# Performance work log

Measured on AMD Instinct MI355X. Metric: run time of the kernel, lower is better.

Reference implementation:

```python
import jax, jax.numpy as jnp
import numpy as np

M, C = 100000, 24
LINE_W, LENGTH_W, REPROJ_W = 0.0, 0.0, 1.0  # forward() default weights


def setup_inputs() -> dict:
    ks = jax.random.split(jax.random.key(0), 8)
    # 3 pole markers per frame, centered ~5m in front of cameras (positive depth)
    pole3d = 0.5 * jax.random.normal(ks[0], (M, 3, 3), jnp.float32) + jnp.array([0.0, 0.0, 5.0], jnp.float32)
    # intrinsics: fx=fy~1000, principal point ~(960,540)
    fx = 1000.0 + 10.0 * jax.random.normal(ks[1], (C,), jnp.float32)
    fy = 1000.0 + 10.0 * jax.random.normal(ks[2], (C,), jnp.float32)
    u0 = 960.0 + 5.0 * jax.random.normal(ks[3], (C,), jnp.float32)
    v0 = 540.0 + 5.0 * jax.random.normal(ks[4], (C,), jnp.float32)
    K = jnp.zeros((C, 3, 3), jnp.float32)
    K = K.at[:, 0, 0].set(fx).at[:, 1, 1].set(fy).at[:, 0, 2].set(u0).at[:, 1, 2].set(v0).at[:, 2, 2].set(1.0)
    dist = 0.01 * jax.random.normal(ks[5], (C, 5), jnp.float32)  # k1,k2,p1,p2,k3
    R = jnp.eye(3, dtype=jnp.float32)[None] + 0.01 * jax.random.normal(ks[6], (C, 3, 3), jnp.float32)
    t = 0.1 * jax.random.normal(ks[7], (C, 3), jnp.float32)
    # detected pixels in a 1920x1080 frame
    pole2d = jax.random.uniform(jax.random.fold_in(ks[0], 1), (M, C, 3, 2), jnp.float32) * jnp.array([1920.0, 1080.0], jnp.float32)
    # visibility mask; guarantee >=1 visible camera per frame (matches non-empty loss_reproj)
    mask = jax.random.randint(jax.random.fold_in(ks[0], 2), (M, C), 0, 2, jnp.int32).at[:, 0].set(1)
    pole = jnp.array([0.5, 0.5], jnp.float32)  # [d1, d2] in meters
    return {"pole3d": pole3d, "pole2d": pole2d, "K": K, "dist": dist, "R": R, "t": t, "pole": pole, "mask": mask}


def _project(X, K, R, t, dist):
    # X: [M,P,3] world points; outputs pixels [M,C,P,2]
    xc = jnp.einsum('cij,mpj->mcpi', R, X) + t[None, :, None, :]   # camera frame
    xn = xc[..., :2] / xc[..., 2:3]                                # perspective divide
    x0, x1 = xn[..., 0], xn[..., 1]
    r2 = x0 * x0 + x1 * x1
    k1, k2, p1, p2, k3 = (dist[:, i][None, :, None] for i in range(5))
    radial = 1.0 + k1 * r2 + k2 * r2 * r2 + k3 * r2 * r2 * r2
    xu = x0 * radial + 2.0 * p1 * x0 * x1 + p2 * (r2 + 2.0 * x0 * x0)
    yu = x1 * radial + p1 * (r2 + 2.0 * x1 * x1) + 2.0 * p2 * x0 * x1
    fx = K[:, 0, 0][None, :, None]; fy = K[:, 1, 1][None, :, None]
    u0 = K[:, 0, 2][None, :, None]; v0 = K[:, 1, 2][None, :, None]
    return jnp.stack([fx * xu + u0, fy * yu + v0], axis=-1)


def reference(pole3d, pole2d, K, dist, R, t, pole, mask):
    d1, d2 = pole[0], pole[1]
    dsum = d1 + d2
    # wand geometry loss per frame
    expect_mid = (d2 * pole3d[:, 0] + d1 * pole3d[:, 2]) / dsum            # [M,3]
    loss_line = jnp.linalg.norm(pole3d[:, 1] - expect_mid, axis=-1)        # [M]
    loss_length = jnp.abs(jnp.linalg.norm(pole3d[:, 0] - pole3d[:, 2], axis=-1) - dsum)
    loss_wand = LINE_W * loss_line + LENGTH_W * loss_length                # [M]
    # reprojection loss
    proj = _project(pole3d, K, R, t, dist)                                 # [M,C,3,2]
    per_cam = REPROJ_W * jnp.linalg.norm(pole2d - proj, axis=-1).mean(axis=-1)  # [M,C]
    m = mask.astype(per_cam.dtype)
    loss_reproj = (per_cam * m).sum(axis=-1) / m.sum(axis=-1)              # masked mean over cams
    return jnp.mean(loss_wand + loss_reproj)
```

## Files before the change

### kernel.cpp

```cpp
#include <hip/hip_runtime.h>

#define MM 100000
#define CC 24
#define BLK 256
#define WPB (BLK / 64)
#define GRID 1280
#define NW (GRID * WPB)
#define NP (MM / 2)

struct Pack {
    float2 a0, a1, a2;
    float  w;
    float  q[9];
};

__device__ __forceinline__ Pack load_pack(
    const float* __restrict__ pole3d, const float* __restrict__ pole2d,
    const int* __restrict__ mask, int m, int c, float active)
{
    Pack pk;
    const float2* pd = (const float2*)(pole2d + ((size_t)m * CC + c) * 6);
    pk.a0 = pd[0]; pk.a1 = pd[1]; pk.a2 = pd[2];
    pk.w = active * (float)mask[(size_t)m * CC + c];
    const float* q = pole3d + (size_t)m * 9;
    #pragma unroll
    for (int i = 0; i < 9; ++i) pk.q[i] = q[i];
    return pk;
}

__global__ __launch_bounds__(BLK) void ba_main_kernel(
    const float* __restrict__ pole3d,
    const float* __restrict__ pole2d,
    const float* __restrict__ Kmat,
    const float* __restrict__ dist,
    const float* __restrict__ Rmat,
    const float* __restrict__ tvec,
    const int*   __restrict__ mask,
    float* __restrict__ ws)
{
    const int tid  = threadIdx.x;
    const int lane = tid & 63;
    const int half = lane >> 5;
    const int cl   = lane & 31;
    const int c    = (cl < CC) ? cl : (CC - 1);
    const float active = (cl < CC) ? 1.f : 0.f;

    const float fx = Kmat[c * 9 + 0], fy = Kmat[c * 9 + 4];
    const float u0 = Kmat[c * 9 + 2], v0 = Kmat[c * 9 + 5];
    const float k1 = dist[c * 5 + 0], k2 = dist[c * 5 + 1];
    const float p1 = dist[c * 5 + 2], p2 = dist[c * 5 + 3], k3 = dist[c * 5 + 4];
    const float r00 = Rmat[c * 9 + 0], r01 = Rmat[c * 9 + 1], r02 = Rmat[c * 9 + 2];
    const float r10 = Rmat[c * 9 + 3], r11 = Rmat[c * 9 + 4], r12 = Rmat[c * 9 + 5];
    const float r20 = Rmat[c * 9 + 6], r21 = Rmat[c * 9 + 7], r22 = Rmat[c * 9 + 8];
    const float t0 = tvec[c * 3 + 0], t1 = tvec[c * 3 + 1], t2 = tvec[c * 3 + 2];

    const int wid = blockIdx.x * WPB + (tid >> 6);

    float acc = 0.f;

    Pack cur = load_pack(pole3d, pole2d, mask, 2 * wid + half, c, active);

    for (int p = wid; p < NP; p += NW) {
        const int pn = p + NW;
        const int pc = (pn < NP) ? pn : wid;
        Pack nxt = load_pack(pole3d, pole2d, mask, 2 * pc + half, c, active);

        float s = 0.f;
        const float2 obs[3] = {cur.a0, cur.a1, cur.a2};
        #pragma unroll
        for (int i = 0; i < 3; ++i) {
            const float X = cur.q[3 * i + 0], Y = cur.q[3 * i + 1], Z = cur.q[3 * i + 2];
            const float xc = r00 * X + r01 * Y + r02 * Z + t0;
            const float yc = r10 * X + r11 * Y + r12 * Z + t1;
            const float zc = r20 * X + r21 * Y + r22 * Z + t2;
            const float inv = __builtin_amdgcn_rcpf(zc);
            const float x0 = xc * inv, x1 = yc * inv;
            const float r2 = x0 * x0 + x1 * x1;
            const float radial = 1.f + r2 * (k1 + r2 * (k2 + r2 * k3));
            const float xu = x0 * radial + 2.f * p1 * x0 * x1 + p2 * (r2 + 2.f * x0 * x0);
            const float yu = x1 * radial + p1 * (r2 + 2.f * x1 * x1) + 2.f * p2 * x0 * x1;
            const float u = fx * xu + u0;
            const float v = fy * yu + v0;
            const float dx = obs[i].x - u;
            const float dy = obs[i].y - v;
            s += __builtin_amdgcn_sqrtf(dx * dx + dy * dy);
        }
        s *= (1.f / 3.f);

        float ss = s * cur.w;
        float ww = cur.w;
        #pragma unroll
        for (int d = 1; d < 32; d <<= 1) {
            ss += __shfl_xor(ss, d);
            ww += __shfl_xor(ww, d);
        }
        acc += ss * __builtin_amdgcn_rcpf(ww);

        cur = nxt;
    }

    float tot = acc + __shfl_xor(acc, 32);

    __shared__ float sh[WPB];
    if (lane == 0) sh[tid >> 6] = tot;
    __syncthreads();
    if (tid == 0) {
        float bl = 0.f;
        #pragma unroll
        for (int j = 0; j < WPB; ++j) bl += sh[j];
        ws[blockIdx.x] = bl;
    }
}

__global__ __launch_bounds__(256) void ba_reduce_kernel(
    const float* __restrict__ ws, float* __restrict__ out)
{
    __shared__ float sh[256];
    float s = 0.f;
    for (int i = threadIdx.x; i < GRID; i += 256) s += ws[i];
    sh[threadIdx.x] = s;
    __syncthreads();
    #pragma unroll
    for (int st = 128; st > 0; st >>= 1) {
        if (threadIdx.x < st) sh[threadIdx.x] += sh[threadIdx.x + st];
        __syncthreads();
    }
    if (threadIdx.x == 0) out[0] = sh[0] * (1.0f / MM);
}

extern "C" void kernel_launch(void* const* d_in, const int* in_sizes, int n_in,
                              void* d_out, int out_size, void* d_ws, size_t ws_size,
                              hipStream_t stream) {
    const float* pole3d = (const float*)d_in[0];
    const float* pole2d = (const float*)d_in[1];
    const float* Kmat   = (const float*)d_in[2];
    const float* dist   = (const float*)d_in[3];
    const float* Rmat   = (const float*)d_in[4];
    const float* tvec   = (const float*)d_in[5];
    const int*   mask   = (const int*)d_in[7];
    float* out = (float*)d_out;
    float* ws  = (float*)d_ws;

    ba_main_kernel<<<GRID, BLK, 0, stream>>>(
        pole3d, pole2d, Kmat, dist, Rmat, tvec, mask, ws);
    ba_reduce_kernel<<<1, 256, 0, stream>>>(ws, out);
}
```

Measured before the change: 28.51 us.

## Share pole3d via bpermute, double-depth prefetch, fuse final reduction with atomic counter

Each lane now loads only one pole3d scalar and the nine coordinates are broadcast within each half-wave via ds_bpermute, cutting redundant loads. The main loop processes two frame-pairs per iteration with two packs prefetched ahead to deepen memory-level parallelism. The separate reduction kernel is replaced by a last-block-done pattern using an atomic counter in workspace, reset by a memset, saving a launch at the cost of an atomic and fences.

```diff
diff --git a/kernel.cpp b/kernel.cpp
--- a/kernel.cpp
+++ b/kernel.cpp
@@ -8,23 +8,19 @@
 #define NW (GRID * WPB)
 #define NP (MM / 2)
 
-struct Pack {
-    float2 a0, a1, a2;
-    float  w;
-    float  q[9];
-};
+struct Pack { float2 a0, a1, a2; float w; float qv; };
 
 __device__ __forceinline__ Pack load_pack(
     const float* __restrict__ pole3d, const float* __restrict__ pole2d,
-    const int* __restrict__ mask, int m, int c, float active)
+    const int* __restrict__ mask, int m, int c, int cl, float active)
 {
     Pack pk;
     const float2* pd = (const float2*)(pole2d + ((size_t)m * CC + c) * 6);
     pk.a0 = pd[0]; pk.a1 = pd[1]; pk.a2 = pd[2];
-    pk.w = active * (float)mask[(size_t)m * CC + c];
-    const float* q = pole3d + (size_t)m * 9;
-    #pragma unroll
-    for (int i = 0; i < 9; ++i) pk.q[i] = q[i];
+    pk.w  = active * (float)mask[(size_t)m * CC + c];
+    float qv = 0.f;
+    if (cl < 9) qv = pole3d[(size_t)m * 9 + cl];
+    pk.qv = qv;
     return pk;
 }
 
@@ -36,7 +32,8 @@
     const float* __restrict__ Rmat,
     const float* __restrict__ tvec,
     const int*   __restrict__ mask,
-    float* __restrict__ ws)
+    float* __restrict__ ws,
+    float* __restrict__ out)
 {
     const int tid  = threadIdx.x;
     const int lane = tid & 63;
@@ -44,6 +41,7 @@
     const int cl   = lane & 31;
     const int c    = (cl < CC) ? cl : (CC - 1);
     const float active = (cl < CC) ? 1.f : 0.f;
+    const int qbase = half * 128;
 
     const float fx = Kmat[c * 9 + 0], fy = Kmat[c * 9 + 4];
     const float u0 = Kmat[c * 9 + 2], v0 = Kmat[c * 9 + 5];
@@ -58,18 +56,17 @@
 
     float acc = 0.f;
 
-    Pack cur = load_pack(pole3d, pole2d, mask, 2 * wid + half, c, active);
-
-    for (int p = wid; p < NP; p += NW) {
-        const int pn = p + NW;
-        const int pc = (pn < NP) ? pn : wid;
-        Pack nxt = load_pack(pole3d, pole2d, mask, 2 * pc + half, c, active);
-
+    auto consume = [&](const Pack& pk) {
+        float q[9];
+        #pragma unroll
+        for (int i = 0; i < 9; ++i)
+            q[i] = __int_as_float(__builtin_amdgcn_ds_bpermute(
+                       qbase + 4 * i, __float_as_int(pk.qv)));
+        const float2 obs[3] = {pk.a0, pk.a1, pk.a2};
         float s = 0.f;
-        const float2 obs[3] = {cur.a0, cur.a1, cur.a2};
         #pragma unroll
         for (int i = 0; i < 3; ++i) {
-            const float X = cur.q[3 * i + 0], Y = cur.q[3 * i + 1], Z = cur.q[3 * i + 2];
+            const float X = q[3 * i + 0], Y = q[3 * i + 1], Z = q[3 * i + 2];
             const float xc = r00 * X + r01 * Y + r02 * Z + t0;
             const float yc = r10 * X + r11 * Y + r12 * Z + t1;
             const float zc = r20 * X + r21 * Y + r22 * Z + t2;
@@ -86,46 +83,55 @@
             s += __builtin_amdgcn_sqrtf(dx * dx + dy * dy);
         }
         s *= (1.f / 3.f);
-
-        float ss = s * cur.w;
-        float ww = cur.w;
+        float ss = s * pk.w, ww = pk.w;
         #pragma unroll
         for (int d = 1; d < 32; d <<= 1) {
             ss += __shfl_xor(ss, d);
             ww += __shfl_xor(ww, d);
         }
         acc += ss * __builtin_amdgcn_rcpf(ww);
+    };
 
-        cur = nxt;
+    Pack c0 = load_pack(pole3d, pole2d, mask, 2 * wid + half, c, cl, active);
+    Pack c1 = load_pack(pole3d, pole2d, mask, 2 * (wid + NW) + half, c, cl, active);
+
+    for (int p = wid; p < NP; p += 2 * NW) {
+        const int p2 = p + 2 * NW, p3 = p + 3 * NW;
+        Pack n0{}, n1{};
+        if (p2 < NP) n0 = load_pack(pole3d, pole2d, mask, 2 * p2 + half, c, cl, active);
+        if (p3 < NP) n1 = load_pack(pole3d, pole2d, mask, 2 * p3 + half, c, cl, active);
+        consume(c0);
+        if (p + NW < NP) consume(c1);
+        c0 = n0; c1 = n1;
     }
 
-    float tot = acc + __shfl_xor(acc, 32);
+    const float tot = acc + __shfl_xor(acc, 32);
 
     __shared__ float sh[WPB];
+    __shared__ int lastFlag;
     if (lane == 0) sh[tid >> 6] = tot;
     __syncthreads();
+
+    float* partials = ws + 64;
     if (tid == 0) {
         float bl = 0.f;
         #pragma unroll
         for (int j = 0; j < WPB; ++j) bl += sh[j];
-        ws[blockIdx.x] = bl;
+        partials[blockIdx.x] = bl;
+        __threadfence();
+        const unsigned prev = atomicAdd((unsigned*)ws, 1u);
+        lastFlag = (prev == GRID - 1);
     }
-}
+    __syncthreads();
 
-__global__ __launch_bounds__(256) void ba_reduce_kernel(
-    const float* __restrict__ ws, float* __restrict__ out)
-{
-    __shared__ float sh[256];
-    float s = 0.f;
-    for (int i = threadIdx.x; i < GRID; i += 256) s += ws[i];
-    sh[threadIdx.x] = s;
-    __syncthreads();
-    #pragma unroll
-    for (int st = 128; st > 0; st >>= 1) {
-        if (threadIdx.x < st) sh[threadIdx.x] += sh[threadIdx.x + st];
-        __syncthreads();
+    if (lastFlag && tid < 64) {
+        __threadfence();
+        float s = 0.f;
+        for (int i = tid; i < GRID; i += 64) s += partials[i];
+        #pragma unroll
+        for (int d = 1; d < 64; d <<= 1) s += __shfl_xor(s, d);
+        if (tid == 0) out[0] = s * (1.0f / MM);
     }
-    if (threadIdx.x == 0) out[0] = sh[0] * (1.0f / MM);
 }
 
 extern "C" void kernel_launch(void* const* d_in, const int* in_sizes, int n_in,
@@ -141,7 +147,8 @@
     float* out = (float*)d_out;
     float* ws  = (float*)d_ws;
 
+    hipMemsetAsync(ws, 0, sizeof(unsigned), stream);
+
     ba_main_kernel<<<GRID, BLK, 0, stream>>>(
-        pole3d, pole2d, Kmat, dist, Rmat, tvec, mask, ws);
-    ba_reduce_kernel<<<1, 256, 0, stream>>>(ws, out);
+        pole3d, pole2d, Kmat, dist, Rmat, tvec, mask, ws, out);
 }
```

Measured after the change: 60.26 us. 111% more time.

## Fuse final reduction via last-block atomic counter and use ballot for mask counts

Applied to the files above, without the earlier changes.

The separate reduce kernel is removed. Each block now writes its partial sum and bumps an atomic counter, and the last block to finish sums all partials and writes the output. The per-frame visible-camera count is taken with a ballot plus popcount instead of a second shuffle reduction. The grid shrinks and launch bounds gain an occupancy hint. A memset is added before the launch to reset the counter, which costs an extra stream operation, and the threadfence/atomic pattern adds a little tail latency.

```diff
diff --git a/kernel.cpp b/kernel.cpp
--- a/kernel.cpp
+++ b/kernel.cpp
@@ -4,7 +4,7 @@
 #define CC 24
 #define BLK 256
 #define WPB (BLK / 64)
-#define GRID 1280
+#define GRID 1024
 #define NW (GRID * WPB)
 #define NP (MM / 2)
 
@@ -21,14 +21,14 @@
     Pack pk;
     const float2* pd = (const float2*)(pole2d + ((size_t)m * CC + c) * 6);
     pk.a0 = pd[0]; pk.a1 = pd[1]; pk.a2 = pd[2];
-    pk.w = active * (float)mask[(size_t)m * CC + c];
+    pk.w  = active * (float)mask[(size_t)m * CC + c];
     const float* q = pole3d + (size_t)m * 9;
     #pragma unroll
     for (int i = 0; i < 9; ++i) pk.q[i] = q[i];
     return pk;
 }
 
-__global__ __launch_bounds__(BLK) void ba_main_kernel(
+__global__ __launch_bounds__(BLK, 4) void ba_main_kernel(
     const float* __restrict__ pole3d,
     const float* __restrict__ pole2d,
     const float* __restrict__ Kmat,
@@ -36,7 +36,8 @@
     const float* __restrict__ Rmat,
     const float* __restrict__ tvec,
     const int*   __restrict__ mask,
-    float* __restrict__ ws)
+    float* __restrict__ ws,
+    float* __restrict__ out)
 {
     const int tid  = threadIdx.x;
     const int lane = tid & 63;
@@ -87,45 +88,47 @@
         }
         s *= (1.f / 3.f);
 
+        const unsigned long long ball = __ballot(cur.w != 0.f);
+        const unsigned wcnt = half ? __popcll(ball >> 32)
+                                   : __popcll(ball & 0xFFFFFFFFull);
+        const float ww = (float)wcnt;
+
         float ss = s * cur.w;
-        float ww = cur.w;
         #pragma unroll
-        for (int d = 1; d < 32; d <<= 1) {
-            ss += __shfl_xor(ss, d);
-            ww += __shfl_xor(ww, d);
-        }
+        for (int d = 1; d < 32; d <<= 1) ss += __shfl_xor(ss, d);
+
         acc += ss * __builtin_amdgcn_rcpf(ww);
 
         cur = nxt;
     }
 
-    float tot = acc + __shfl_xor(acc, 32);
+    const float tot = acc + __shfl_xor(acc, 32);
 
     __shared__ float sh[WPB];
+    __shared__ int lastFlag;
     if (lane == 0) sh[tid >> 6] = tot;
     __syncthreads();
+
+    float* partials = ws + 64;
     if (tid == 0) {
         float bl = 0.f;
         #pragma unroll
         for (int j = 0; j < WPB; ++j) bl += sh[j];
-        ws[blockIdx.x] = bl;
+        partials[blockIdx.x] = bl;
+        __threadfence();
+        const unsigned prev = atomicAdd((unsigned*)ws, 1u);
+        lastFlag = (prev == GRID - 1);
     }
-}
+    __syncthreads();
 
-__global__ __launch_bounds__(256) void ba_reduce_kernel(
-    const float* __restrict__ ws, float* __restrict__ out)
-{
-    __shared__ float sh[256];
-    float s = 0.f;
-    for (int i = threadIdx.x; i < GRID; i += 256) s += ws[i];
-    sh[threadIdx.x] = s;
-    __syncthreads();
-    #pragma unroll
-    for (int st = 128; st > 0; st >>= 1) {
-        if (threadIdx.x < st) sh[threadIdx.x] += sh[threadIdx.x + st];
-        __syncthreads();
+    if (lastFlag && tid < 64) {
+        __threadfence();
+        float s = 0.f;
+        for (int i = tid; i < GRID; i += 64) s += partials[i];
+        #pragma unroll
+        for (int d = 1; d < 64; d <<= 1) s += __shfl_xor(s, d);
+        if (tid == 0) out[0] = s * (1.0f / MM);
     }
-    if (threadIdx.x == 0) out[0] = sh[0] * (1.0f / MM);
 }
 
 extern "C" void kernel_launch(void* const* d_in, const int* in_sizes, int n_in,
@@ -141,7 +144,8 @@
     float* out = (float*)d_out;
     float* ws  = (float*)d_ws;
 
+    hipMemsetAsync(ws, 0, sizeof(unsigned), stream);
+
     ba_main_kernel<<<GRID, BLK, 0, stream>>>(
-        pole3d, pole2d, Kmat, dist, Rmat, tvec, mask, ws);
-    ba_reduce_kernel<<<1, 256, 0, stream>>>(ws, out);
+        pole3d, pole2d, Kmat, dist, Rmat, tvec, mask, ws, out);
 }
```

Result: slower. 62.27 us (+118.4%).
